# Kernel tuning notes

Hardware: AMD Instinct MI355X
Metric: run time of the kernel (lower is better)

The kernel has to match this reference:

```python
import jax, jax.numpy as jnp
import numpy as np
import math

D_MODEL = 1024
D_STATE = 128
EXPAND = 2
HEADDIM = 64
NGROUPS = 1
ROPE_FRACTION = 0.5
A_FLOOR = 1e-4
D_INNER = EXPAND * D_MODEL            # 2048
NHEADS = D_INNER // HEADDIM           # 32
SPLIT = int(D_STATE * ROPE_FRACTION)  # 64
R = SPLIT // 2                        # 32 rotary angles; rotary applied to first R state dims
D_IN_PROJ = 2 * D_INNER + 2 * D_STATE * NGROUPS + 3 * NHEADS + R  # 4480
BATCH = 1
SEQLEN = 1024


def setup_inputs() -> dict:
    key = jax.random.key(0)
    k0, k1, k2, k3 = jax.random.split(key, 4)
    u = jax.random.normal(k0, (BATCH, SEQLEN, D_MODEL), jnp.float32)
    w_in = jax.random.normal(k1, (D_IN_PROJ, D_MODEL), jnp.float32) * (D_MODEL ** -0.5)
    w_out = jax.random.normal(k2, (D_MODEL, D_INNER), jnp.float32) * (D_INNER ** -0.5)
    # dt_bias init matches torch: inverse-softplus of dt ~ LogUniform(dt_min, dt_max)
    dt = jnp.exp(jax.random.uniform(k3, (NHEADS,), jnp.float32)
                 * (math.log(0.1) - math.log(0.001)) + math.log(0.001))
    dt = jnp.maximum(dt, 1e-4)
    dt_bias = dt + jnp.log(-jnp.expm1(-dt))
    D = jnp.ones((NHEADS,), jnp.float32)
    return {"u": u, "w_in": w_in, "w_out": w_out, "dt_bias": dt_bias, "D": D}


def _mamba3_forward(u, w_in, w_out, dt_bias, D):
    b, l, _ = u.shape
    proj = u @ w_in.T  # [b, l, D_IN_PROJ]
    sizes = [D_INNER, D_INNER, D_STATE * NGROUPS, D_STATE * NGROUPS, NHEADS, NHEADS, NHEADS, R]
    idx = np.cumsum(sizes)[:-1]
    z, x, B, C, dd_dt, dd_A, trap, angles = jnp.split(proj, idx, axis=-1)

    A = jnp.minimum(-jax.nn.softplus(dd_A), -A_FLOOR)      # [b,l,h]
    dt = jax.nn.softplus(dd_dt + dt_bias)                  # [b,l,h]
    tr = jax.nn.sigmoid(trap)                              # [b,l,h]
    # rotary angle: tanh(angles)[b,l,1,R] * dt[b,l,h,1] * pi, cumsum over time
    theta = jnp.cumsum(jnp.tanh(angles)[:, :, None, :] * dt[..., None] * jnp.pi, axis=1)  # [b,l,h,R]

    x_h = x.reshape(b, l, NHEADS, HEADDIM)
    z_h = z.reshape(b, l, NHEADS, HEADDIM)
    B_h = B.reshape(b, l, NGROUPS, D_STATE)[:, :, 0, :]  # only group 0 is read in the loop
    C_h = C.reshape(b, l, NGROUPS, D_STATE)[:, :, 0, :]

    def step(carry, inp):
        sr, si, px = carry  # sr: [b,h,p,n], si: [b,h,p,R] (imag beyond R is identically zero)
        dt_t, A_t, tr_t, th, bt, ct, xt = inp
        alpha = jnp.exp(A_t * dt_t)[:, :, None, None]          # [b,h,1,1]
        beta = ((1.0 - tr_t) * dt_t)[:, :, None, None] * alpha
        gamma = (tr_t * dt_t)[:, :, None, None]
        base = bt[:, None, None, :] * (px[..., None] * beta + xt[..., None] * gamma)  # [b,h,p,n]
        rc = jnp.cos(th)[:, :, None, :]  # [b,h,1,R]
        rs = jnp.sin(th)[:, :, None, :]
        sr = sr * alpha + jnp.concatenate([base[..., :R] * rc, base[..., R:]], axis=-1)
        si = si * alpha + base[..., :R] * rs
        ctb = ct[:, None, None, :]
        y = (jnp.sum((sr[..., :R] * rc + si * rs) * ctb[..., :R], axis=-1)
             + jnp.sum(sr[..., R:] * ctb[..., R:], axis=-1))  # [b,h,p]
        return (sr, si, xt), y

    sr0 = jnp.zeros((b, NHEADS, HEADDIM, D_STATE), u.dtype)
    si0 = jnp.zeros((b, NHEADS, HEADDIM, R), u.dtype)
    px0 = jnp.zeros((b, NHEADS, HEADDIM), u.dtype)
    xs = (jnp.moveaxis(dt, 1, 0), jnp.moveaxis(A, 1, 0), jnp.moveaxis(tr, 1, 0),
          jnp.moveaxis(theta, 1, 0), jnp.moveaxis(B_h, 1, 0), jnp.moveaxis(C_h, 1, 0),
          jnp.moveaxis(x_h, 1, 0))
    _, ys = jax.lax.scan(step, (sr0, si0, px0), xs)  # [l,b,h,p]
    y = jnp.moveaxis(ys, 0, 1) + D[None, None, :, None] * x_h
    out = y * jax.nn.silu(z_h)
    return out.reshape(b, l, D_INNER) @ w_out.T


def reference(u, w_in, w_out, dt_bias, D):
    return _mamba3_forward(u, w_in, w_out, dt_bias, D)
```

## Files before the change

kernel.cpp:

```cpp
#include <hip/hip_runtime.h>
#include <math.h>

#define L_SEQ   1024
#define DMODEL  1024
#define DINNER  2048
#define NH      32
#define HD      64
#define NS      160
#define RR      32
#define NPROJ   4480
#define OFF_Z   0
#define OFF_X   2048
#define OFF_B   4096
#define OFF_C   4224
#define OFF_DT  4352
#define OFF_A   4384
#define OFF_TR  4416
#define OFF_ANG 4448
#define NC      16
#define CL      64
#define PIF     3.14159265358979323846f

typedef __attribute__((ext_vector_type(8))) short bf16x8;
typedef __attribute__((ext_vector_type(4))) float f32x4;
typedef unsigned int u32;
typedef unsigned short u16;

__device__ __forceinline__ float softplusf(float x) {
  return (x > 20.f) ? x : log1pf(expf(x));
}
__device__ __forceinline__ u16 f2bf(float f) {
  u32 u = __float_as_uint(f);
  u32 r = (u + 0x7FFFu + ((u >> 16) & 1u)) >> 16;
  return (u16)r;
}
__device__ __forceinline__ float bf2f(u16 v) {
  return __uint_as_float(((u32)v) << 16);
}

__device__ __forceinline__ void gload_lds16(const u16* g, u16* l) {
  __builtin_amdgcn_global_load_lds(
      (const __attribute__((address_space(1))) u32*)(unsigned long long)(const void*)g,
      (__attribute__((address_space(3))) u32*)(unsigned long long)(void*)l, 16, 0, 0);
}

__global__ __launch_bounds__(256) void cvt2_bf16(
    const float* __restrict__ s0, u16* __restrict__ d0, int q0,
    const float* __restrict__ s1, u16* __restrict__ d1, int q1) {
  int i = blockIdx.x * 256 + threadIdx.x;
  const float* s; u16* d; int j;
  if (i < q0) { s = s0; d = d0; j = i; }
  else { j = i - q0; if (j >= q1) return; s = s1; d = d1; }
  const float4* s4 = (const float4*)s;
  float4 a = s4[2 * j], b = s4[2 * j + 1];
  union { u16 h[8]; uint4 v; } o;
  o.h[0] = f2bf(a.x); o.h[1] = f2bf(a.y); o.h[2] = f2bf(a.z); o.h[3] = f2bf(a.w);
  o.h[4] = f2bf(b.x); o.h[5] = f2bf(b.y); o.h[6] = f2bf(b.z); o.h[7] = f2bf(b.w);
  ((uint4*)d)[j] = o.v;
}

template <int BM, int BN>
__global__ __launch_bounds__(256) void gemm_bf16(
    const u16* __restrict__ A, const u16* __restrict__ B,
    float* __restrict__ C, int N, int K) {
  constexpr int BK = 32;
  constexpr int WM = BM / 2, WN = BN / 2;
  constexpr int MF = WM / 16, NF = WN / 16;
  constexpr int CA = BM / 64;
  constexpr int CB = BN / 64;
  __shared__ u16 lds[(BM + BN) * BK];

  const int bm = blockIdx.y * BM, bn = blockIdx.x * BN;
  const int tid = threadIdx.x, w = tid >> 6, lane = tid & 63;
  const int wr = w >> 1, wc = w & 1;
  const int fr = lane & 15, sl = lane >> 4;
  const int lrow = lane >> 2, lslot = (lane & 3) * 8;

  const u16* gA[CA]; u16* lA[CA];
#pragma unroll
  for (int j = 0; j < CA; ++j) {
    int ca = w * CA + j;
    gA[j] = A + (size_t)(bm + ca * 16 + lrow) * K + lslot;
    lA[j] = lds + ca * 512;
  }
  const u16* gB[CB]; u16* lB[CB];
#pragma unroll
  for (int j = 0; j < CB; ++j) {
    int cb = w * CB + j;
    gB[j] = B + (size_t)(bn + cb * 16 + lrow) * K + lslot;
    lB[j] = lds + BM * 32 + cb * 512;
  }

  const u16* aptr[MF]; const u16* bptr[NF];
#pragma unroll
  for (int i = 0; i < MF; ++i)
    aptr[i] = lds + (wr * WM + i * 16 + fr) * 32 + sl * 8;
#pragma unroll
  for (int j = 0; j < NF; ++j)
    bptr[j] = lds + BM * 32 + (wc * WN + j * 16 + fr) * 32 + sl * 8;

  f32x4 acc[MF][NF] = {};
  const int iters = K / BK;

#pragma unroll
  for (int j = 0; j < CA; ++j) gload_lds16(gA[j], lA[j]);
#pragma unroll
  for (int j = 0; j < CB; ++j) gload_lds16(gB[j], lB[j]);

  for (int it = 0; it < iters; ++it) {
    __syncthreads();
    bf16x8 af[MF], bfv[NF];
#pragma unroll
    for (int i = 0; i < MF; ++i) af[i] = *(const bf16x8*)aptr[i];
#pragma unroll
    for (int j = 0; j < NF; ++j) bfv[j] = *(const bf16x8*)bptr[j];
    __syncthreads();
    if (it + 1 < iters) {
#pragma unroll
      for (int j = 0; j < CA; ++j) gload_lds16(gA[j] + (it + 1) * BK, lA[j]);
#pragma unroll
      for (int j = 0; j < CB; ++j) gload_lds16(gB[j] + (it + 1) * BK, lB[j]);
    }
#pragma unroll
    for (int i = 0; i < MF; ++i)
#pragma unroll
      for (int j = 0; j < NF; ++j)
        acc[i][j] = __builtin_amdgcn_mfma_f32_16x16x32_bf16(
            af[i], bfv[j], acc[i][j], 0, 0, 0);
  }

#pragma unroll
  for (int i = 0; i < MF; ++i) {
    int rb = bm + wr * WM + i * 16 + sl * 4;
#pragma unroll
    for (int j = 0; j < NF; ++j) {
      int cb = bn + wc * WN + j * 16 + fr;
#pragma unroll
      for (int r = 0; r < 4; ++r)
        C[(size_t)(rb + r) * N + cb] = acc[i][j][r];
    }
  }
}

__global__ __launch_bounds__(256) void prep_scalars_cvt(
    const float* __restrict__ proj, const float* __restrict__ dt_bias,
    float* __restrict__ dtA, float* __restrict__ lnaA,
    float* __restrict__ betaA, float* __restrict__ gammaA,
    float* __restrict__ angP,
    const float* __restrict__ wsrc, u16* __restrict__ wdst) {
  const int b = blockIdx.x;
  if (b < 1024) {
    int j = b * 256 + threadIdx.x;
    const float4* s4 = (const float4*)wsrc;
    float4 a = s4[2 * j], bb = s4[2 * j + 1];
    union { u16 h[8]; uint4 v; } o;
    o.h[0] = f2bf(a.x); o.h[1] = f2bf(a.y); o.h[2] = f2bf(a.z); o.h[3] = f2bf(a.w);
    o.h[4] = f2bf(bb.x); o.h[5] = f2bf(bb.y); o.h[6] = f2bf(bb.z); o.h[7] = f2bf(bb.w);
    ((uint4*)wdst)[j] = o.v;
    return;
  }
  int idx = (b - 1024) * 256 + threadIdx.x;
  int h = idx & 31, l = idx >> 5;
  const float* prow = proj + (size_t)l * NPROJ;
  float dt = softplusf(prow[OFF_DT + h] + dt_bias[h]);
  float Apos = fmaxf(softplusf(prow[OFF_A + h]), 1e-4f);
  float tr = 1.f / (1.f + expf(-prow[OFF_TR + h]));
  float lna = -Apos * dt;
  float alpha = expf(lna);
  dtA[idx] = dt;
  lnaA[idx] = lna;
  betaA[idx] = (1.f - tr) * dt * alpha;
  gammaA[idx] = tr * dt;
  angP[idx] = tanhf(prow[OFF_ANG + h]) * PIF;
}

__global__ __launch_bounds__(256) void theta_scan(
    const float* __restrict__ angP, const float* __restrict__ dtA,
    float* __restrict__ rc, float* __restrict__ rs) {
  const int h = blockIdx.x >> 5;
  const int r = blockIdx.x & 31;
  const int tid = threadIdx.x;
  __shared__ float ldssc[256];

  float csum[4];
  float run = 0.f;
#pragma unroll
  for (int i = 0; i < 4; ++i) {
    int l = tid * 4 + i;
    run += angP[l * NH + r] * dtA[l * NH + h];
    csum[i] = run;
  }
  ldssc[tid] = run;
  __syncthreads();
  for (int off = 1; off < 256; off <<= 1) {
    float t = (tid >= off) ? ldssc[tid - off] : 0.f;
    __syncthreads();
    ldssc[tid] += t;
    __syncthreads();
  }
  float excl = ldssc[tid] - run;
#pragma unroll
  for (int i = 0; i < 4; ++i) {
    int l = tid * 4 + i;
    float th = excl + csum[i];
    size_t o = ((size_t)l * NH + h) * RR + r;
    rc[o] = cosf(th);
    rs[o] = sinf(th);
  }
}

__global__ __launch_bounds__(256) void uvgA(
    const float* __restrict__ proj, const float* __restrict__ betaA,
    const float* __restrict__ gammaA, const float* __restrict__ lnaA,
    const float* __restrict__ rc, const float* __restrict__ rs,
    u16* __restrict__ U, u16* __restrict__ V, u16* __restrict__ Gt,
    float* __restrict__ cumA, float* __restrict__ adec,
    u16* __restrict__ S) {
  const int h = blockIdx.x >> 4, c = blockIdx.x & 15;
  const int c0 = c * CL;
  const int tid = threadIdx.x;
  const int w = tid >> 6, lane = tid & 63;

  __shared__ __attribute__((aligned(16))) char smem[54784];
  u16 (*Gw)[72]   = (u16(*)[72])(smem);
  float* wsc      = (float*)(smem + 9216);
  float* bet      = (float*)(smem + 9472);
  float* gam      = (float*)(smem + 9728);
  float (*xs)[64] = (float(*)[64])(smem + 10240);
  u16 (*Vl)[168]  = (u16(*)[168])(smem + 10240);
  u16 (*Vt)[72]   = (u16(*)[72])(smem + 31744);

  if (w < 3) {
    for (int i = tid; i < 65 * 16; i += 192) {
      int r = i >> 4, c4 = i & 15;
      int l = c0 - 1 + r;
      float4 v = {0.f, 0.f, 0.f, 0.f};
      if (l >= 0)
        v = *(const float4*)(proj + (size_t)l * NPROJ + OFF_X + h * HD + c4 * 4);
      *(float4*)&xs[r][c4 * 4] = v;
    }
  } else {
    const int t = lane;
    float v = lnaA[(c0 + t) * NH + h];
#pragma unroll
    for (int k = 1; k < 64; k <<= 1) {
      int src = t - k;
      float o = __shfl(v, src < 0 ? 0 : src);
      if (t >= k) v += o;
    }
    cumA[(size_t)h * L_SEQ + c0 + t] = v;
    if (t == 63) adec[h * NC + c] = expf(v);
    float c63 = __shfl(v, 63);
    wsc[t] = expf(c63 - v);
    bet[t] = betaA[(c0 + t) * NH + h];
    gam[t] = gammaA[(c0 + t) * NH + h];
  }
  __syncthreads();

  {
    const int p = lane;
    union { u16 hh[16]; uint4 q[2]; } og, ow;
    float xprev = xs[w * 16][p];
#pragma unroll
    for (int i = 0; i < 16; ++i) {
      int s = w * 16 + i;
      float xcur = xs[s + 1][p];
      float g = bet[s] * xprev + gam[s] * xcur;
      og.hh[i] = f2bf(g);
      ow.hh[i] = f2bf(g * wsc[s]);
      xprev = xcur;
    }
    uint4* gdst = (uint4*)(Gt + (((size_t)h * NC + c) * HD + p) * CL + w * 16);
    gdst[0] = og.q[0];
    gdst[1] = og.q[1];
    *(uint4*)&Gw[p][w * 16] = ow.q[0];
    *(uint4*)&Gw[p][w * 16 + 8] = ow.q[1];
  }
  __syncthreads();

  if (tid < 160) {
    const int n = tid;
    const int idxB = (n < 64) ? (n & 31) : (n - 32);
    const bool is_re = (n < 32);
    const bool has_rot = (n < 64);
    for (int ss = 0; ss < 64; ++ss) {
      int l = c0 + ss;
      const float* prow = proj + (size_t)l * NPROJ;
      float Bv = prow[OFF_B + idxB];
      float Cv = prow[OFF_C + idxB];
      if (has_rot) {
        float rv = is_re ? rc[((size_t)l * NH + h) * RR + idxB]
                         : rs[((size_t)l * NH + h) * RR + idxB];
        Bv *= rv; Cv *= rv;
      }
      u16 bb = f2bf(Bv);
      U[((size_t)h * L_SEQ + l) * NS + n] = f2bf(Cv);
      V[((size_t)h * L_SEQ + l) * NS + n] = bb;
      Vl[ss][n] = bb;
    }
  }
  __syncthreads();

  if (tid < 160) {
    int n = tid;
#pragma unroll
    for (int s2 = 0; s2 < 32; ++s2) {
      u32 lo = Vl[2 * s2][n], hi = Vl[2 * s2 + 1][n];
      *(u32*)&Vt[n][2 * s2] = lo | (hi << 16);
    }
  }
  __syncthreads();

  const int wr = w >> 1, wc = w & 1;
  const int fr = lane & 15, sl = lane >> 4;
  f32x4 acc[2][5] = {};
#pragma unroll
  for (int ks = 0; ks < 2; ++ks) {
    bf16x8 a0 = *(const bf16x8*)&Gw[wr * 32 + fr][ks * 32 + sl * 8];
    bf16x8 a1 = *(const bf16x8*)&Gw[wr * 32 + 16 + fr][ks * 32 + sl * 8];
    bf16x8 bv[5];
#pragma unroll
    for (int fj = 0; fj < 5; ++fj)
      bv[fj] = *(const bf16x8*)&Vt[wc * 80 + fj * 16 + fr][ks * 32 + sl * 8];
#pragma unroll
    for (int fj = 0; fj < 5; ++fj) {
      acc[0][fj] = __builtin_amdgcn_mfma_f32_16x16x32_bf16(a0, bv[fj], acc[0][fj], 0, 0, 0);
      acc[1][fj] = __builtin_amdgcn_mfma_f32_16x16x32_bf16(a1, bv[fj], acc[1][fj], 0, 0, 0);
    }
  }
  u16* Fb = S + (size_t)(c * NH + h) * HD * NS;
#pragma unroll
  for (int fi = 0; fi < 2; ++fi)
#pragma unroll
    for (int fj = 0; fj < 5; ++fj)
#pragma unroll
      for (int r = 0; r < 4; ++r) {
        int p = wr * 32 + fi * 16 + sl * 4 + r;
        int n = wc * 80 + fj * 16 + fr;
        Fb[(size_t)p * NS + n] = f2bf(acc[fi][fj][r]);
      }
}

__global__ __launch_bounds__(256) void combine(
    u16* __restrict__ S, const float* __restrict__ adec) {
  const int idx = blockIdx.x * 256 + threadIdx.x;
  if (idx >= NH * HD * NS) return;
  const int n = idx % NS;
  const int rem = idx / NS;
  const int p = rem & 63;
  const int h = rem >> 6;
  float F = 0.f;
  for (int c = 0; c < NC; ++c) {
    size_t off = ((size_t)(c * NH + h) * HD + p) * NS + n;
    float sv = bf2f(S[off]);
    S[off] = f2bf(F);
    F = fmaf(F, adec[h * NC + c], sv);
  }
}

__global__ __launch_bounds__(256) void passB(
    const float* __restrict__ proj, const u16* __restrict__ U,
    const u16* __restrict__ V, const u16* __restrict__ Gt,
    const float* __restrict__ cumA, const u16* __restrict__ S,
    const float* __restrict__ Dvec, u16* __restrict__ yz) {
  const int c = blockIdx.x >> 5, h = blockIdx.x & 31;
  const int c0 = c * CL;
  const int tid = threadIdx.x;
  const int w = tid >> 6, lane = tid & 63;
  const int wr = w >> 1, wc = w & 1;
  const int fr = lane & 15, sl = lane >> 4;
  __shared__ u16 Ul[64][168];
  __shared__ u16 BB[64][168];
  __shared__ u16 Ml[64][72];
  __shared__ u16 Gl[64][72];
  __shared__ float cums[64], ecum[64];

  const u16* Us = U + ((size_t)h * L_SEQ + c0) * NS;
  for (int i = tid; i < 1280; i += 256) {
    int r = i / 20, ch = i % 20;
    *(uint4*)&Ul[r][ch * 8] = *(const uint4*)(Us + (size_t)r * NS + ch * 8);
  }
  {
    const u16* S0 = S + (size_t)(c * NH + h) * HD * NS;
    for (int i = tid; i < 1280; i += 256) {
      int r = i / 20, ch = i % 20;
      *(uint4*)&BB[r][ch * 8] = *(const uint4*)(S0 + (size_t)r * NS + ch * 8);
    }
  }
  if (tid < 64) {
    float cv = cumA[(size_t)h * L_SEQ + c0 + tid];
    cums[tid] = cv;
    ecum[tid] = expf(cv);
  }
  __syncthreads();

  f32x4 acc[2][2] = {};
#pragma unroll
  for (int ks = 0; ks < 5; ++ks) {
    bf16x8 a0 = *(const bf16x8*)&Ul[wr * 32 + fr][ks * 32 + sl * 8];
    bf16x8 a1 = *(const bf16x8*)&Ul[wr * 32 + 16 + fr][ks * 32 + sl * 8];
    bf16x8 b0 = *(const bf16x8*)&BB[wc * 32 + fr][ks * 32 + sl * 8];
    bf16x8 b1 = *(const bf16x8*)&BB[wc * 32 + 16 + fr][ks * 32 + sl * 8];
    acc[0][0] = __builtin_amdgcn_mfma_f32_16x16x32_bf16(a0, b0, acc[0][0], 0, 0, 0);
    acc[0][1] = __builtin_amdgcn_mfma_f32_16x16x32_bf16(a0, b1, acc[0][1], 0, 0, 0);
    acc[1][0] = __builtin_amdgcn_mfma_f32_16x16x32_bf16(a1, b0, acc[1][0], 0, 0, 0);
    acc[1][1] = __builtin_amdgcn_mfma_f32_16x16x32_bf16(a1, b1, acc[1][1], 0, 0, 0);
  }
#pragma unroll
  for (int fi = 0; fi < 2; ++fi)
#pragma unroll
    for (int fj = 0; fj < 2; ++fj)
#pragma unroll
      for (int r = 0; r < 4; ++r)
        acc[fi][fj][r] *= ecum[wr * 32 + fi * 16 + sl * 4 + r];
  __syncthreads();

  const u16* Vs = V + ((size_t)h * L_SEQ + c0) * NS;
  for (int i = tid; i < 1280; i += 256) {
    int r = i / 20, ch = i % 20;
    *(uint4*)&BB[r][ch * 8] = *(const uint4*)(Vs + (size_t)r * NS + ch * 8);
  }
  const u16* Gs = Gt + ((size_t)h * NC + c) * HD * CL;
  for (int i = tid; i < 512; i += 256) {
    int p = i >> 3, ch = i & 7;
    *(uint4*)&Gl[p][ch * 8] = *(const uint4*)(Gs + (size_t)p * CL + ch * 8);
  }
  __syncthreads();

  f32x4 pac[2][2] = {};
#pragma unroll
  for (int ks = 0; ks < 5; ++ks) {
    bf16x8 a0 = *(const bf16x8*)&Ul[wr * 32 + fr][ks * 32 + sl * 8];
    bf16x8 a1 = *(const bf16x8*)&Ul[wr * 32 + 16 + fr][ks * 32 + sl * 8];
    bf16x8 b0 = *(const bf16x8*)&BB[wc * 32 + fr][ks * 32 + sl * 8];
    bf16x8 b1 = *(const bf16x8*)&BB[wc * 32 + 16 + fr][ks * 32 + sl * 8];
    pac[0][0] = __builtin_amdgcn_mfma_f32_16x16x32_bf16(a0, b0, pac[0][0], 0, 0, 0);
    pac[0][1] = __builtin_amdgcn_mfma_f32_16x16x32_bf16(a0, b1, pac[0][1], 0, 0, 0);
    pac[1][0] = __builtin_amdgcn_mfma_f32_16x16x32_bf16(a1, b0, pac[1][0], 0, 0, 0);
    pac[1][1] = __builtin_amdgcn_mfma_f32_16x16x32_bf16(a1, b1, pac[1][1], 0, 0, 0);
  }
#pragma unroll
  for (int fi = 0; fi < 2; ++fi)
#pragma unroll
    for (int fj = 0; fj < 2; ++fj)
#pragma unroll
      for (int r = 0; r < 4; ++r) {
        int t = wr * 32 + fi * 16 + sl * 4 + r;
        int ss = wc * 32 + fj * 16 + fr;
        float m = (ss <= t) ? expf(cums[t] - cums[ss]) * pac[fi][fj][r] : 0.f;
        Ml[t][ss] = f2bf(m);
      }
  __syncthreads();

#pragma unroll
  for (int ks = 0; ks < 2; ++ks) {
    bf16x8 a0 = *(const bf16x8*)&Ml[wr * 32 + fr][ks * 32 + sl * 8];
    bf16x8 a1 = *(const bf16x8*)&Ml[wr * 32 + 16 + fr][ks * 32 + sl * 8];
    bf16x8 b0 = *(const bf16x8*)&Gl[wc * 32 + fr][ks * 32 + sl * 8];
    bf16x8 b1 = *(const bf16x8*)&Gl[wc * 32 + 16 + fr][ks * 32 + sl * 8];
    acc[0][0] = __builtin_amdgcn_mfma_f32_16x16x32_bf16(a0, b0, acc[0][0], 0, 0, 0);
    acc[0][1] = __builtin_amdgcn_mfma_f32_16x16x32_bf16(a0, b1, acc[0][1], 0, 0, 0);
    acc[1][0] = __builtin_amdgcn_mfma_f32_16x16x32_bf16(a1, b0, acc[1][0], 0, 0, 0);
    acc[1][1] = __builtin_amdgcn_mfma_f32_16x16x32_bf16(a1, b1, acc[1][1], 0, 0, 0);
  }

  const float Dh = Dvec[h];
#pragma unroll
  for (int fi = 0; fi < 2; ++fi)
#pragma unroll
    for (int fj = 0; fj < 2; ++fj)
#pragma unroll
      for (int r = 0; r < 4; ++r) {
        int t = wr * 32 + fi * 16 + sl * 4 + r;
        int p = wc * 32 + fj * 16 + fr;
        int l = c0 + t;
        float x = proj[(size_t)l * NPROJ + OFF_X + h * HD + p];
        float z = proj[(size_t)l * NPROJ + OFF_Z + h * HD + p];
        float y = acc[fi][fj][r] + Dh * x;
        float sg = z / (1.f + expf(-z));
        yz[(size_t)l * DINNER + h * HD + p] = f2bf(y * sg);
      }
}

extern "C" void kernel_launch(void* const* d_in, const int* in_sizes, int n_in,
                              void* d_out, int out_size, void* d_ws, size_t ws_size,
                              hipStream_t stream) {
  const float* u       = (const float*)d_in[0];
  const float* w_in    = (const float*)d_in[1];
  const float* w_out   = (const float*)d_in[2];
  const float* dt_bias = (const float*)d_in[3];
  const float* Dvec    = (const float*)d_in[4];
  float* out = (float*)d_out;

  float* ws = (float*)d_ws;
  float* proj   = ws;
  float* dtA    = proj + 4587520;
  float* lnaA   = dtA + 32768;
  float* betaA  = lnaA + 32768;
  float* gammaA = betaA + 32768;
  float* cumA   = gammaA + 32768;
  float* adec   = cumA + 32768;
  float* angP   = adec + 512;
  float* rcb    = angP + 32768;
  float* rsb    = rcb + 1048576;
  u16*   Sb     = (u16*)(rsb + 1048576);
  u16*   Gtb    = Sb + 5242880;
  u16*   Ubuf   = Gtb + 2097152;
  u16*   Vbuf   = Ubuf + 5242880;
  u16*   yzb    = Vbuf + 5242880;
  u16*   wob    = yzb + 2097152;
  u16*   ub     = Ubuf;
  u16*   wib    = Ubuf + 1048576;

  cvt2_bf16<<<(131072 + 573440) / 256, 256, 0, stream>>>(
      u, ub, 131072, w_in, wib, 573440);

  gemm_bf16<128, 128><<<dim3(NPROJ / 128, L_SEQ / 128), 256, 0, stream>>>(
      ub, wib, proj, NPROJ, DMODEL);

  prep_scalars_cvt<<<1024 + 128, 256, 0, stream>>>(
      proj, dt_bias, dtA, lnaA, betaA, gammaA, angP, w_out, wob);

  theta_scan<<<NH * RR, 256, 0, stream>>>(angP, dtA, rcb, rsb);

  uvgA<<<NH * NC, 256, 0, stream>>>(
      proj, betaA, gammaA, lnaA, rcb, rsb, Ubuf, Vbuf, Gtb, cumA, adec, Sb);

  combine<<<(NH * HD * NS + 255) / 256, 256, 0, stream>>>(Sb, adec);

  passB<<<NC * NH, 256, 0, stream>>>(
      proj, Ubuf, Vbuf, Gtb, cumA, Sb, Dvec, yzb);

  gemm_bf16<64, 64><<<dim3(DMODEL / 64, L_SEQ / 64), 256, 0, stream>>>(
      yzb, wob, out, DMODEL, DINNER);
}
```

Baseline: 133.9 us.

## Recompute U/V/G in passB, swizzle GEMM LDS, shrink in-proj tile

The uvgA kernel no longer writes the rotated B/C (U, V) and G intermediates to global memory. passB recomputes them from proj, rc/rs and beta/gamma in shared memory, which cuts global writes and re-reads at the cost of redundant rotary and G computation. The bf16 GEMM now XOR-swizzles its LDS slot layout to reduce bank conflicts. The input projection GEMM uses 64x128 tiles for more blocks. The passB intra-chunk and inter-chunk matmuls are reordered so the BB buffer can be reused.

```diff
diff --git a/kernel.cpp b/kernel.cpp
--- a/kernel.cpp
+++ b/kernel.cpp
@@ -74,7 +74,8 @@
   const int tid = threadIdx.x, w = tid >> 6, lane = tid & 63;
   const int wr = w >> 1, wc = w & 1;
   const int fr = lane & 15, sl = lane >> 4;
-  const int lrow = lane >> 2, lslot = (lane & 3) * 8;
+  const int lrow = lane >> 2;
+  const int lslot = ((lane & 3) ^ ((lrow >> 1) & 3)) * 8;
 
   const u16* gA[CA]; u16* lA[CA];
 #pragma unroll
@@ -91,13 +92,14 @@
     lB[j] = lds + BM * 32 + cb * 512;
   }
 
+  const int rsl = (sl ^ ((fr >> 1) & 3)) * 8;
   const u16* aptr[MF]; const u16* bptr[NF];
 #pragma unroll
   for (int i = 0; i < MF; ++i)
-    aptr[i] = lds + (wr * WM + i * 16 + fr) * 32 + sl * 8;
+    aptr[i] = lds + (wr * WM + i * 16 + fr) * 32 + rsl;
 #pragma unroll
   for (int j = 0; j < NF; ++j)
-    bptr[j] = lds + BM * 32 + (wc * WN + j * 16 + fr) * 32 + sl * 8;
+    bptr[j] = lds + BM * 32 + (wc * WN + j * 16 + fr) * 32 + rsl;
 
   f32x4 acc[MF][NF] = {};
   const int iters = K / BK;
@@ -213,7 +215,6 @@
     const float* __restrict__ proj, const float* __restrict__ betaA,
     const float* __restrict__ gammaA, const float* __restrict__ lnaA,
     const float* __restrict__ rc, const float* __restrict__ rs,
-    u16* __restrict__ U, u16* __restrict__ V, u16* __restrict__ Gt,
     float* __restrict__ cumA, float* __restrict__ adec,
     u16* __restrict__ S) {
   const int h = blockIdx.x >> 4, c = blockIdx.x & 15;
@@ -259,22 +260,150 @@
 
   {
     const int p = lane;
-    union { u16 hh[16]; uint4 q[2]; } og, ow;
+    union { u16 hh[16]; uint4 q[2]; } ow;
     float xprev = xs[w * 16][p];
 #pragma unroll
     for (int i = 0; i < 16; ++i) {
       int s = w * 16 + i;
       float xcur = xs[s + 1][p];
       float g = bet[s] * xprev + gam[s] * xcur;
-      og.hh[i] = f2bf(g);
       ow.hh[i] = f2bf(g * wsc[s]);
       xprev = xcur;
     }
-    uint4* gdst = (uint4*)(Gt + (((size_t)h * NC + c) * HD + p) * CL + w * 16);
-    gdst[0] = og.q[0];
-    gdst[1] = og.q[1];
     *(uint4*)&Gw[p][w * 16] = ow.q[0];
     *(uint4*)&Gw[p][w * 16 + 8] = ow.q[1];
+  }
+  __syncthreads();
+
+  if (tid < 160) {
+    const int n = tid;
+    const int idxB = (n < 64) ? (n & 31) : (n - 32);
+    const bool is_re = (n < 32);
+    const bool has_rot = (n < 64);
+    for (int ss = 0; ss < 64; ++ss) {
+      int l = c0 + ss;
+      float Bv = proj[(size_t)l * NPROJ + OFF_B + idxB];
+      if (has_rot) {
+        float rv = is_re ? rc[((size_t)l * NH + h) * RR + idxB]
+                         : rs[((size_t)l * NH + h) * RR + idxB];
+        Bv *= rv;
+      }
+      Vl[ss][n] = f2bf(Bv);
+    }
+  }
+  __syncthreads();
+
+  if (tid < 160) {
+    int n = tid;
+#pragma unroll
+    for (int s2 = 0; s2 < 32; ++s2) {
+      u32 lo = Vl[2 * s2][n], hi = Vl[2 * s2 + 1][n];
+      *(u32*)&Vt[n][2 * s2] = lo | (hi << 16);
+    }
+  }
+  __syncthreads();
+
+  const int wr = w >> 1, wc = w & 1;
+  const int fr = lane & 15, sl = lane >> 4;
+  f32x4 acc[2][5] = {};
+#pragma unroll
+  for (int ks = 0; ks < 2; ++ks) {
+    bf16x8 a0 = *(const bf16x8*)&Gw[wr * 32 + fr][ks * 32 + sl * 8];
+    bf16x8 a1 = *(const bf16x8*)&Gw[wr * 32 + 16 + fr][ks * 32 + sl * 8];
+    bf16x8 bv[5];
+#pragma unroll
+    for (int fj = 0; fj < 5; ++fj)
+      bv[fj] = *(const bf16x8*)&Vt[wc * 80 + fj * 16 + fr][ks * 32 + sl * 8];
+#pragma unroll
+    for (int fj = 0; fj < 5; ++fj) {
+      acc[0][fj] = __builtin_amdgcn_mfma_f32_16x16x32_bf16(a0, bv[fj], acc[0][fj], 0, 0, 0);
+      acc[1][fj] = __builtin_amdgcn_mfma_f32_16x16x32_bf16(a1, bv[fj], acc[1][fj], 0, 0, 0);
+    }
+  }
+  u16* Fb = S + (size_t)(c * NH + h) * HD * NS;
+#pragma unroll
+  for (int fi = 0; fi < 2; ++fi)
+#pragma unroll
+    for (int fj = 0; fj < 5; ++fj)
+#pragma unroll
+      for (int r = 0; r < 4; ++r) {
+        int p = wr * 32 + fi * 16 + sl * 4 + r;
+        int n = wc * 80 + fj * 16 + fr;
+        Fb[(size_t)p * NS + n] = f2bf(acc[fi][fj][r]);
+      }
+}
+
+__global__ __launch_bounds__(256) void combine(
+    u16* __restrict__ S, const float* __restrict__ adec) {
+  const int idx = blockIdx.x * 256 + threadIdx.x;
+  if (idx >= NH * HD * NS) return;
+  const int n = idx % NS;
+  const int rem = idx / NS;
+  const int p = rem & 63;
+  const int h = rem >> 6;
+  float F = 0.f;
+  for (int c = 0; c < NC; ++c) {
+    size_t off = ((size_t)(c * NH + h) * HD + p) * NS + n;
+    float sv = bf2f(S[off]);
+    S[off] = f2bf(F);
+    F = fmaf(F, adec[h * NC + c], sv);
+  }
+}
+
+__global__ __launch_bounds__(256) void passB(
+    const float* __restrict__ proj, const float* __restrict__ rc,
+    const float* __restrict__ rs, const float* __restrict__ betaA,
+    const float* __restrict__ gammaA, const float* __restrict__ cumA,
+    const u16* __restrict__ S, const float* __restrict__ Dvec,
+    u16* __restrict__ yz) {
+  const int c = blockIdx.x >> 5, h = blockIdx.x & 31;
+  const int c0 = c * CL;
+  const int tid = threadIdx.x;
+  const int w = tid >> 6, lane = tid & 63;
+  const int wr = w >> 1, wc = w & 1;
+  const int fr = lane & 15, sl = lane >> 4;
+
+  __shared__ __attribute__((aligned(16))) char smem[62464];
+  u16 (*Ul)[168] = (u16(*)[168])(smem);
+  u16 (*BB)[168] = (u16(*)[168])(smem + 21504);
+  u16 (*Ml)[72]  = (u16(*)[72]) (smem + 43008);
+  u16 (*Gl)[72]  = (u16(*)[72]) (smem + 52224);
+  float* cums = (float*)(smem + 61440);
+  float* ecum = (float*)(smem + 61696);
+  float* bet  = (float*)(smem + 61952);
+  float* gam  = (float*)(smem + 62208);
+  float (*xs)[64] = (float(*)[64])smem;
+
+  for (int i = tid; i < 65 * 16; i += 256) {
+    int r = i >> 4, c4 = i & 15;
+    int l = c0 - 1 + r;
+    float4 v = {0.f, 0.f, 0.f, 0.f};
+    if (l >= 0)
+      v = *(const float4*)(proj + (size_t)l * NPROJ + OFF_X + h * HD + c4 * 4);
+    *(float4*)&xs[r][c4 * 4] = v;
+  }
+  if (tid < 64) {
+    float cv = cumA[(size_t)h * L_SEQ + c0 + tid];
+    cums[tid] = cv;
+    ecum[tid] = expf(cv);
+    bet[tid] = betaA[(c0 + tid) * NH + h];
+    gam[tid] = gammaA[(c0 + tid) * NH + h];
+  }
+  __syncthreads();
+
+  {
+    const int p = lane;
+    union { u16 hh[16]; uint4 q[2]; } og;
+    float xprev = xs[w * 16][p];
+#pragma unroll
+    for (int i = 0; i < 16; ++i) {
+      int s = w * 16 + i;
+      float xcur = xs[s + 1][p];
+      og.hh[i] = f2bf(bet[s] * xprev + gam[s] * xcur);
+      xprev = xcur;
+    }
+    *(uint4*)&Gl[p][w * 16] = og.q[0];
+    *(uint4*)&Gl[p][w * 16 + 8] = og.q[1];
   }
   __syncthreads();
 
@@ -293,137 +422,9 @@
                          : rs[((size_t)l * NH + h) * RR + idxB];
         Bv *= rv; Cv *= rv;
       }
-      u16 bb = f2bf(Bv);
-      U[((size_t)h * L_SEQ + l) * NS + n] = f2bf(Cv);
-      V[((size_t)h * L_SEQ + l) * NS + n] = bb;
-      Vl[ss][n] = bb;
-    }
-  }
-  __syncthreads();
-
-  if (tid < 160) {
-    int n = tid;
-#pragma unroll
-    for (int s2 = 0; s2 < 32; ++s2) {
-      u32 lo = Vl[2 * s2][n], hi = Vl[2 * s2 + 1][n];
-      *(u32*)&Vt[n][2 * s2] = lo | (hi << 16);
-    }
-  }
-  __syncthreads();
-
-  const int wr = w >> 1, wc = w & 1;
-  const int fr = lane & 15, sl = lane >> 4;
-  f32x4 acc[2][5] = {};
-#pragma unroll
-  for (int ks = 0; ks < 2; ++ks) {
-    bf16x8 a0 = *(const bf16x8*)&Gw[wr * 32 + fr][ks * 32 + sl * 8];
-    bf16x8 a1 = *(const bf16x8*)&Gw[wr * 32 + 16 + fr][ks * 32 + sl * 8];
-    bf16x8 bv[5];
-#pragma unroll
-    for (int fj = 0; fj < 5; ++fj)
-      bv[fj] = *(const bf16x8*)&Vt[wc * 80 + fj * 16 + fr][ks * 32 + sl * 8];
-#pragma unroll
-    for (int fj = 0; fj < 5; ++fj) {
-      acc[0][fj] = __builtin_amdgcn_mfma_f32_16x16x32_bf16(a0, bv[fj], acc[0][fj], 0, 0, 0);
-      acc[1][fj] = __builtin_amdgcn_mfma_f32_16x16x32_bf16(a1, bv[fj], acc[1][fj], 0, 0, 0);
-    }
-  }
-  u16* Fb = S + (size_t)(c * NH + h) * HD * NS;
-#pragma unroll
-  for (int fi = 0; fi < 2; ++fi)
-#pragma unroll
-    for (int fj = 0; fj < 5; ++fj)
-#pragma unroll
-      for (int r = 0; r < 4; ++r) {
-        int p = wr * 32 + fi * 16 + sl * 4 + r;
-        int n = wc * 80 + fj * 16 + fr;
-        Fb[(size_t)p * NS + n] = f2bf(acc[fi][fj][r]);
-      }
-}
-
-__global__ __launch_bounds__(256) void combine(
-    u16* __restrict__ S, const float* __restrict__ adec) {
-  const int idx = blockIdx.x * 256 + threadIdx.x;
-  if (idx >= NH * HD * NS) return;
-  const int n = idx % NS;
-  const int rem = idx / NS;
-  const int p = rem & 63;
-  const int h = rem >> 6;
-  float F = 0.f;
-  for (int c = 0; c < NC; ++c) {
-    size_t off = ((size_t)(c * NH + h) * HD + p) * NS + n;
-    float sv = bf2f(S[off]);
-    S[off] = f2bf(F);
-    F = fmaf(F, adec[h * NC + c], sv);
-  }
-}
-
-__global__ __launch_bounds__(256) void passB(
-    const float* __restrict__ proj, const u16* __restrict__ U,
-    const u16* __restrict__ V, const u16* __restrict__ Gt,
-    const float* __restrict__ cumA, const u16* __restrict__ S,
-    const float* __restrict__ Dvec, u16* __restrict__ yz) {
-  const int c = blockIdx.x >> 5, h = blockIdx.x & 31;
-  const int c0 = c * CL;
-  const int tid = threadIdx.x;
-  const int w = tid >> 6, lane = tid & 63;
-  const int wr = w >> 1, wc = w & 1;
-  const int fr = lane & 15, sl = lane >> 4;
-  __shared__ u16 Ul[64][168];
-  __shared__ u16 BB[64][168];
-  __shared__ u16 Ml[64][72];
-  __shared__ u16 Gl[64][72];
-  __shared__ float cums[64], ecum[64];
-
-  const u16* Us = U + ((size_t)h * L_SEQ + c0) * NS;
-  for (int i = tid; i < 1280; i += 256) {
-    int r = i / 20, ch = i % 20;
-    *(uint4*)&Ul[r][ch * 8] = *(const uint4*)(Us + (size_t)r * NS + ch * 8);
-  }
-  {
-    const u16* S0 = S + (size_t)(c * NH + h) * HD * NS;
-    for (int i = tid; i < 1280; i += 256) {
-      int r = i / 20, ch = i % 20;
-      *(uint4*)&BB[r][ch * 8] = *(const uint4*)(S0 + (size_t)r * NS + ch * 8);
-    }
-  }
-  if (tid < 64) {
-    float cv = cumA[(size_t)h * L_SEQ + c0 + tid];
-    cums[tid] = cv;
-    ecum[tid] = expf(cv);
-  }
-  __syncthreads();
-
-  f32x4 acc[2][2] = {};
-#pragma unroll
-  for (int ks = 0; ks < 5; ++ks) {
-    bf16x8 a0 = *(const bf16x8*)&Ul[wr * 32 + fr][ks * 32 + sl * 8];
-    bf16x8 a1 = *(const bf16x8*)&Ul[wr * 32 + 16 + fr][ks * 32 + sl * 8];
-    bf16x8 b0 = *(const bf16x8*)&BB[wc * 32 + fr][ks * 32 + sl * 8];
-    bf16x8 b1 = *(const bf16x8*)&BB[wc * 32 + 16 + fr][ks * 32 + sl * 8];
-    acc[0][0] = __builtin_amdgcn_mfma_f32_16x16x32_bf16(a0, b0, acc[0][0], 0, 0, 0);
-    acc[0][1] = __builtin_amdgcn_mfma_f32_16x16x32_bf16(a0, b1, acc[0][1], 0, 0, 0);
-    acc[1][0] = __builtin_amdgcn_mfma_f32_16x16x32_bf16(a1, b0, acc[1][0], 0, 0, 0);
-    acc[1][1] = __builtin_amdgcn_mfma_f32_16x16x32_bf16(a1, b1, acc[1][1], 0, 0, 0);
-  }
-#pragma unroll
-  for (int fi = 0; fi < 2; ++fi)
-#pragma unroll
-    for (int fj = 0; fj < 2; ++fj)
-#pragma unroll
-      for (int r = 0; r < 4; ++r)
-        acc[fi][fj][r] *= ecum[wr * 32 + fi * 16 + sl * 4 + r];
-  __syncthreads();
-
-  const u16* Vs = V + ((size_t)h * L_SEQ + c0) * NS;
-  for (int i = tid; i < 1280; i += 256) {
-    int r = i / 20, ch = i % 20;
-    *(uint4*)&BB[r][ch * 8] = *(const uint4*)(Vs + (size_t)r * NS + ch * 8);
-  }
-  const u16* Gs = Gt + ((size_t)h * NC + c) * HD * CL;
-  for (int i = tid; i < 512; i += 256) {
-    int p = i >> 3, ch = i & 7;
-    *(uint4*)&Gl[p][ch * 8] = *(const uint4*)(Gs + (size_t)p * CL + ch * 8);
+      Ul[ss][n] = f2bf(Cv);
+      BB[ss][n] = f2bf(Bv);
+    }
   }
   __syncthreads();
 
@@ -452,6 +453,7 @@
       }
   __syncthreads();
 
+  f32x4 acc[2][2] = {};
 #pragma unroll
   for (int ks = 0; ks < 2; ++ks) {
     bf16x8 a0 = *(const bf16x8*)&Ml[wr * 32 + fr][ks * 32 + sl * 8];
@@ -463,6 +465,29 @@
     acc[1][0] = __builtin_amdgcn_mfma_f32_16x16x32_bf16(a1, b0, acc[1][0], 0, 0, 0);
     acc[1][1] = __builtin_amdgcn_mfma_f32_16x16x32_bf16(a1, b1, acc[1][1], 0, 0, 0);
   }
+  __syncthreads();
+
+  {
+    const u16* S0 = S + (size_t)(c * NH + h) * HD * NS;
+    for (int i = tid; i < 1280; i += 256) {
+      int r = i / 20, ch = i % 20;
+      *(uint4*)&BB[r][ch * 8] = *(const uint4*)(S0 + (size_t)r * NS + ch * 8);
+    }
+  }
+  __syncthreads();
+
+  f32x4 p2[2][2] = {};
+#pragma unroll
+  for (int ks = 0; ks < 5; ++ks) {
+    bf16x8 a0 = *(const bf16x8*)&Ul[wr * 32 + fr][ks * 32 + sl * 8];
+    bf16x8 a1 = *(const bf16x8*)&Ul[wr * 32 + 16 + fr][ks * 32 + sl * 8];
+    bf16x8 b0 = *(const bf16x8*)&BB[wc * 32 + fr][ks * 32 + sl * 8];
+    bf16x8 b1 = *(const bf16x8*)&BB[wc * 32 + 16 + fr][ks * 32 + sl * 8];
+    p2[0][0] = __builtin_amdgcn_mfma_f32_16x16x32_bf16(a0, b0, p2[0][0], 0, 0, 0);
+    p2[0][1] = __builtin_amdgcn_mfma_f32_16x16x32_bf16(a0, b1, p2[0][1], 0, 0, 0);
+    p2[1][0] = __builtin_amdgcn_mfma_f32_16x16x32_bf16(a1, b0, p2[1][0], 0, 0, 0);
+    p2[1][1] = __builtin_amdgcn_mfma_f32_16x16x32_bf16(a1, b1, p2[1][1], 0, 0, 0);
+  }
 
   const float Dh = Dvec[h];
 #pragma unroll
@@ -474,9 +499,10 @@
         int t = wr * 32 + fi * 16 + sl * 4 + r;
         int p = wc * 32 + fj * 16 + fr;
         int l = c0 + t;
+        float y = acc[fi][fj][r] + p2[fi][fj][r] * ecum[t];
         float x = proj[(size_t)l * NPROJ + OFF_X + h * HD + p];
         float z = proj[(size_t)l * NPROJ + OFF_Z + h * HD + p];
-        float y = acc[fi][fj][r] + Dh * x;
+        y += Dh * x;
         float sg = z / (1.f + expf(-z));
         yz[(size_t)l * DINNER + h * HD + p] = f2bf(y * sg);
       }
@@ -504,18 +530,15 @@
   float* rcb    = angP + 32768;
   float* rsb    = rcb + 1048576;
   u16*   Sb     = (u16*)(rsb + 1048576);
-  u16*   Gtb    = Sb + 5242880;
-  u16*   Ubuf   = Gtb + 2097152;
-  u16*   Vbuf   = Ubuf + 5242880;
-  u16*   yzb    = Vbuf + 5242880;
+  u16*   yzb    = Sb + 5242880;
   u16*   wob    = yzb + 2097152;
-  u16*   ub     = Ubuf;
-  u16*   wib    = Ubuf + 1048576;
+  u16*   ub     = Sb;
+  u16*   wib    = Sb + 1048576;
 
   cvt2_bf16<<<(131072 + 573440) / 256, 256, 0, stream>>>(
       u, ub, 131072, w_in, wib, 573440);
 
-  gemm_bf16<128, 128><<<dim3(NPROJ / 128, L_SEQ / 128), 256, 0, stream>>>(
+  gemm_bf16<64, 128><<<dim3(NPROJ / 128, L_SEQ / 64), 256, 0, stream>>>(
       ub, wib, proj, NPROJ, DMODEL);
 
   prep_scalars_cvt<<<1024 + 128, 256, 0, stream>>>(
@@ -524,12 +547,12 @@
   theta_scan<<<NH * RR, 256, 0, stream>>>(angP, dtA, rcb, rsb);
 
   uvgA<<<NH * NC, 256, 0, stream>>>(
-      proj, betaA, gammaA, lnaA, rcb, rsb, Ubuf, Vbuf, Gtb, cumA, adec, Sb);
+      proj, betaA, gammaA, lnaA, rcb, rsb, cumA, adec, Sb);
 
   combine<<<(NH * HD * NS + 255) / 256, 256, 0, stream>>>(Sb, adec);
 
   passB<<<NC * NH, 256, 0, stream>>>(
-      proj, Ubuf, Vbuf, Gtb, cumA, Sb, Dvec, yzb);
+      proj, rcb, rsb, betaA, gammaA, cumA, Sb, Dvec, yzb);
 
   gemm_bf16<64, 64><<<dim3(DMODEL / 64, L_SEQ / 64), 256, 0, stream>>>(
       yzb, wob, out, DMODEL, DINNER);
```

Measured after the change: 147.5 us. 10.1% more time.
